# Kernel tuning notes

Hardware: AMD Instinct MI355X
Metric: run time of the kernel (lower is better)

## Reference

```python
import jax, jax.numpy as jnp
import numpy as np

NUM_HEADS = 16

def _stablemax3_s(x):
    # 3rd-order Taylor approx of exp(x), Eq 38
    pos = 1.0 + x * (1.0 + 0.5 * x * (1.0 + x / 3.0))
    neg = 1.0 / (1.0 - x * (1.0 - 0.5 * x * (1.0 - x / 3.0)))
    return jnp.where(x >= 0, pos, neg)

def stablemax3(logits, axis=-1):
    logits = logits - jnp.max(logits, axis=axis, keepdims=True)
    s = _stablemax3_s(logits)
    return s / jnp.sum(s, axis=axis, keepdims=True)

def setup_inputs() -> dict:
    key = jax.random.key(0)
    k1, k2, k3 = jax.random.split(key, 3)
    B, S, D = 2, 2048, 1024
    x = jax.random.normal(k1, (B, S, D), dtype=jnp.float32)
    w_qkv = jax.random.normal(k2, (3 * D, D), dtype=jnp.float32) * 0.02
    w_out = jax.random.normal(k3, (D, D), dtype=jnp.float32) * 0.02
    b_out = jnp.zeros((D,), dtype=jnp.float32)
    return {"x": x, "w_qkv": w_qkv, "w_out": w_out, "b_out": b_out}

def reference(x, w_qkv, w_out, b_out):
    B, S, D = x.shape
    H = NUM_HEADS
    hd = D // H
    scale = hd ** (-0.5)
    qkv = x @ w_qkv.T                                  # [B, S, 3D]
    qkv = qkv.reshape(B, S, 3, H, hd)
    qkv = jnp.transpose(qkv, (2, 0, 3, 1, 4))          # [3, B, H, S, hd]
    q, k, v = qkv[0], qkv[1], qkv[2]                   # pos(.) is identity here
    attn = jnp.einsum('bhsd,bhtd->bhst', q, k) * scale # [B, H, S, S]
    attn = stablemax3(attn, axis=-1)
    out = jnp.einsum('bhst,bhtd->bhsd', attn, v)       # [B, H, S, hd]
    out = jnp.transpose(out, (0, 2, 1, 3)).reshape(B, S, D)
    return out @ w_out.T + b_out
```

## Files before the change

kernel.cpp:

```cpp
#include <hip/hip_runtime.h>

typedef _Float16 half8 __attribute__((ext_vector_type(8)));
typedef _Float16 half4 __attribute__((ext_vector_type(4)));
typedef _Float16 half2v __attribute__((ext_vector_type(2)));
typedef float floatx4 __attribute__((ext_vector_type(4)));
typedef unsigned int uint2v __attribute__((ext_vector_type(2)));
typedef unsigned int uint4v __attribute__((ext_vector_type(4)));

__device__ __forceinline__ void gl_lds16(const _Float16* g, _Float16* l) {
    __builtin_amdgcn_global_load_lds(
        (const __attribute__((address_space(1))) void*)g,
        (__attribute__((address_space(3))) void*)l, 16, 0, 0);
}

__device__ __forceinline__ half2v cvt_pk(float a, float b) {
    return __builtin_bit_cast(half2v, __builtin_amdgcn_cvt_pkrtz(a, b));
}

__device__ __forceinline__ half2v rcp2(half2v d) {
#if __has_builtin(__builtin_amdgcn_rcph)
    half2v r;
    r[0] = __builtin_amdgcn_rcph(d[0]);
    r[1] = __builtin_amdgcn_rcph(d[1]);
    return r;
#else
    half2v r;
    r[0] = (_Float16)__builtin_amdgcn_rcpf((float)d[0]);
    r[1] = (_Float16)__builtin_amdgcn_rcpf((float)d[1]);
    return r;
#endif
}

__device__ __forceinline__ float dot2acc(half2v a, float acc) {
#if __has_builtin(__builtin_amdgcn_fdot2)
    const half2v one = {(_Float16)1.0f, (_Float16)1.0f};
    return __builtin_amdgcn_fdot2(a, one, acc, false);
#else
    return acc + (float)a[0] + (float)a[1];
#endif
}

__device__ __forceinline__ half8 from4(half2v a, half2v b, half2v c, half2v d) {
    uint4v u = {__builtin_bit_cast(unsigned int, a), __builtin_bit_cast(unsigned int, b),
                __builtin_bit_cast(unsigned int, c), __builtin_bit_cast(unsigned int, d)};
    return __builtin_bit_cast(half8, u);
}

__device__ __forceinline__ half8 from_lohi(half4 lo, half4 hi) {
    uint2v l = __builtin_bit_cast(uint2v, lo);
    uint2v h = __builtin_bit_cast(uint2v, hi);
    uint4v u = {l[0], l[1], h[0], h[1]};
    return __builtin_bit_cast(half8, u);
}

__global__ __launch_bounds__(256) void cvt_xw(const floatx4* __restrict__ x,
                                              const floatx4* __restrict__ wq,
                                              half4* __restrict__ xh,
                                              half4* __restrict__ wqh) {
    int i = blockIdx.x * 256 + threadIdx.x;
    floatx4 v;
    half4 h;
    if (i < 1048576) {
        v = x[i];
#pragma unroll
        for (int j = 0; j < 4; ++j) h[j] = (_Float16)v[j];
        xh[i] = h;
    } else {
        int j4 = i - 1048576;
        v = wq[j4];
#pragma unroll
        for (int j = 0; j < 4; ++j) h[j] = (_Float16)v[j];
        wqh[j4] = h;
    }
}

__global__ __launch_bounds__(256) void cvt_f32_f16(const floatx4* __restrict__ in,
                                                   half4* __restrict__ out, int n4) {
    int i = blockIdx.x * 256 + threadIdx.x;
    if (i >= n4) return;
    floatx4 v = in[i];
    half4 h;
#pragma unroll
    for (int j = 0; j < 4; ++j) h[j] = (_Float16)v[j];
    out[i] = h;
}

__global__ __launch_bounds__(256) void gemm_qkv(const _Float16* __restrict__ A,
                                                const _Float16* __restrict__ B,
                                                _Float16* __restrict__ qh,
                                                _Float16* __restrict__ kh,
                                                _Float16* __restrict__ vth) {
    const int K = 1024;
    __shared__ _Float16 SH[128 * 68];
    _Float16* As = SH;
    _Float16* Bs = SH + 4096;
    const int t = threadIdx.x;
    const int lane = t & 63, w = t >> 6;
    const int l15 = lane & 15, quad = lane >> 4;
    const int wm = w >> 1, wn = w & 1;
    const int m0 = blockIdx.y * 128, n0 = blockIdx.x * 128;

    floatx4 acc[4][4];
    const floatx4 zf = {0.f, 0.f, 0.f, 0.f};
#pragma unroll
    for (int i = 0; i < 4; ++i)
#pragma unroll
        for (int j = 0; j < 4; ++j) acc[i][j] = zf;

    for (int kt = 0; kt < K; kt += 32) {
        __syncthreads();
#pragma unroll
        for (int it = 0; it < 2; ++it) {
            int cc = it * 256 + t;
            int row = cc >> 2, kc = cc & 3;
            gl_lds16(&A[(size_t)(m0 + row) * K + kt + kc * 8], &As[cc * 8]);
            gl_lds16(&B[(size_t)(n0 + row) * K + kt + kc * 8], &Bs[cc * 8]);
        }
        __syncthreads();
        half8 af[4], bfr[4];
#pragma unroll
        for (int i = 0; i < 4; ++i)
            af[i] = *(const half8*)&As[(wm * 64 + i * 16 + l15) * 32 + quad * 8];
#pragma unroll
        for (int i = 0; i < 4; ++i)
            bfr[i] = *(const half8*)&Bs[(wn * 64 + i * 16 + l15) * 32 + quad * 8];
#pragma unroll
        for (int mi = 0; mi < 4; ++mi)
#pragma unroll
            for (int ni = 0; ni < 4; ++ni)
                acc[mi][ni] = __builtin_amdgcn_mfma_f32_16x16x32_f16(af[mi], bfr[ni],
                                                                     acc[mi][ni], 0, 0, 0);
    }

    const int b = m0 >> 11, s0 = m0 & 2047;
#pragma unroll
    for (int hf = 0; hf < 2; ++hf) {
        __syncthreads();
        if (wn == hf) {
#pragma unroll
            for (int mi = 0; mi < 4; ++mi)
#pragma unroll
                for (int ni = 0; ni < 4; ++ni)
#pragma unroll
                    for (int r = 0; r < 4; ++r)
                        SH[(wm * 64 + mi * 16 + quad * 4 + r) * 68 + ni * 16 + l15] =
                            (_Float16)acc[mi][ni][r];
        }
        __syncthreads();
        const int cbase = n0 + hf * 64;
        if (n0 < 2048) {
            const int hh = (cbase & 1023) >> 6;
            _Float16* dst = (n0 < 1024 ? qh : kh) + (size_t)((b << 4) | hh) * 131072;
#pragma unroll
            for (int it = 0; it < 4; ++it) {
                int cc = it * 256 + t;
                int r = cc >> 3, c8 = cc & 7;
                half4 lo = *(const half4*)&SH[r * 68 + c8 * 8];
                half4 hi = *(const half4*)&SH[r * 68 + c8 * 8 + 4];
                *(half8*)&dst[(size_t)(s0 + r) * 64 + c8 * 8] = from_lohi(lo, hi);
            }
        } else {
            const int hh = (cbase - 2048) >> 6;
            _Float16* dst = vth + (size_t)((b << 4) | hh) * 131072;
#pragma unroll
            for (int it = 0; it < 4; ++it) {
                int cc = it * 256 + t;
                int d = cc >> 4, s8 = cc & 15;
                half8 v;
#pragma unroll
                for (int j = 0; j < 8; ++j) v[j] = SH[(s8 * 8 + j) * 68 + d];
                *(half8*)&dst[(size_t)d * 2048 + s0 + s8 * 8] = v;
            }
        }
    }
}

__global__ __launch_bounds__(256) void gemm_out(const _Float16* __restrict__ A,
                                                const _Float16* __restrict__ B,
                                                float* __restrict__ C,
                                                const float* __restrict__ bias) {
    const int K = 1024, N = 1024;
    __shared__ _Float16 SH[6144];
    _Float16* As = SH;
    _Float16* Bs = SH + 2048;
    const int t = threadIdx.x;
    const int lane = t & 63, w = t >> 6;
    const int l15 = lane & 15, quad = lane >> 4;
    const int wm = w >> 1, wn = w & 1;
    const int m0 = blockIdx.y * 64, n0 = blockIdx.x * 128;

    floatx4 acc[2][4];
    const floatx4 zf = {0.f, 0.f, 0.f, 0.f};
#pragma unroll
    for (int i = 0; i < 2; ++i)
#pragma unroll
        for (int j = 0; j < 4; ++j) acc[i][j] = zf;

    for (int kt = 0; kt < K; kt += 32) {
        __syncthreads();
        {
            int row = t >> 2, kc = t & 3;
            gl_lds16(&A[(size_t)(m0 + row) * K + kt + kc * 8], &As[t * 8]);
        }
#pragma unroll
        for (int it = 0; it < 2; ++it) {
            int cc = it * 256 + t;
            int row = cc >> 2, kc = cc & 3;
            gl_lds16(&B[(size_t)(n0 + row) * K + kt + kc * 8], &Bs[cc * 8]);
        }
        __syncthreads();
        half8 af[2], bfr[4];
#pragma unroll
        for (int i = 0; i < 2; ++i)
            af[i] = *(const half8*)&As[(wm * 32 + i * 16 + l15) * 32 + quad * 8];
#pragma unroll
        for (int i = 0; i < 4; ++i)
            bfr[i] = *(const half8*)&Bs[(wn * 64 + i * 16 + l15) * 32 + quad * 8];
#pragma unroll
        for (int mi = 0; mi < 2; ++mi)
#pragma unroll
            for (int ni = 0; ni < 4; ++ni)
                acc[mi][ni] = __builtin_amdgcn_mfma_f32_16x16x32_f16(af[mi], bfr[ni],
                                                                     acc[mi][ni], 0, 0, 0);
    }

#pragma unroll
    for (int mi = 0; mi < 2; ++mi) {
#pragma unroll
        for (int ni = 0; ni < 4; ++ni) {
            int col = n0 + wn * 64 + ni * 16 + l15;
            float bv = bias[col];
#pragma unroll
            for (int r = 0; r < 4; ++r) {
                int row = m0 + wm * 32 + mi * 16 + quad * 4 + r;
                C[(size_t)row * N + col] = acc[mi][ni][r] + bv;
            }
        }
    }
}

__global__ __launch_bounds__(256) void attn_kernel(const _Float16* __restrict__ qh,
                                                   const _Float16* __restrict__ kh,
                                                   const _Float16* __restrict__ vth,
                                                   _Float16* __restrict__ out) {
    __shared__ _Float16 SM[16384];

    const int t = threadIdx.x;
    const int lane = t & 63, w = t >> 6;
    const int l15 = lane & 15, quad = lane >> 4;
    const int sw = l15 & 7;
    const int q0 = blockIdx.x * 128;
    const int bh = blockIdx.y;
    const int b = bh >> 4, h = bh & 15;

    const _Float16* Qp = qh + (size_t)bh * 131072 + q0 * 64;
    const _Float16* Kp = kh + (size_t)bh * 131072;
    const _Float16* VTp = vth + (size_t)bh * 131072;

    const int row0 = t >> 3, cg0 = (t & 7) ^ (row0 & 7);
    const int row1 = 32 + row0, cg1 = (t & 7) ^ (row1 & 7);
    const _Float16* K0 = &Kp[(size_t)row0 * 64 + cg0 * 8];
    const _Float16* K1 = &Kp[(size_t)row1 * 64 + cg1 * 8];
    const _Float16* V0 = &VTp[(size_t)row0 * 2048 + cg0 * 8];
    const _Float16* V1 = &VTp[(size_t)row1 * 2048 + cg1 * 8];

    const floatx4 zf = {0.f, 0.f, 0.f, 0.f};

    half8 qf[2][2];
#pragma unroll
    for (int nh = 0; nh < 2; ++nh)
#pragma unroll
        for (int kk = 0; kk < 2; ++kk) {
            half8 q = *(const half8*)&Qp[(w * 32 + nh * 16 + l15) * 64 + kk * 32 + quad * 8];
#pragma unroll
            for (int j = 0; j < 8; ++j) q[j] = q[j] * (_Float16)0.125f;
            qf[nh][kk] = q;
        }

    float rmax[2] = {-1.0e30f, -1.0e30f};
    gl_lds16(K0, &SM[t * 8]);
    gl_lds16(K1, &SM[2048 + t * 8]);
    __syncthreads();
    for (int kt = 0, cur = 0; kt < 2048; kt += 64, cur ^= 1) {
        if (kt + 64 < 2048) {
            _Float16* kd = cur ? &SM[0] : &SM[4096];
            gl_lds16(K0 + (size_t)(kt + 64) * 64, kd + t * 8);
            gl_lds16(K1 + (size_t)(kt + 64) * 64, kd + 2048 + t * 8);
        }
        const _Float16* Ks = cur ? &SM[4096] : &SM[0];
        floatx4 sa[4][2];
#pragma unroll
        for (int T = 0; T < 4; ++T) { sa[T][0] = zf; sa[T][1] = zf; }
#pragma unroll
        for (int kk = 0; kk < 2; ++kk) {
            half8 kf[4];
#pragma unroll
            for (int T = 0; T < 4; ++T)
                kf[T] = *(const half8*)&Ks[((T * 16 + l15) << 6) +
                                           ((((kk << 2) + quad) ^ sw) << 3)];
            __builtin_amdgcn_s_setprio(1);
#pragma unroll
            for (int T = 0; T < 4; ++T)
#pragma unroll
                for (int nh = 0; nh < 2; ++nh)
                    sa[T][nh] = __builtin_amdgcn_mfma_f32_16x16x32_f16(kf[T], qf[nh][kk],
                                                                      sa[T][nh], 0, 0, 0);
            __builtin_amdgcn_s_setprio(0);
        }
#pragma unroll
        for (int T = 0; T < 4; ++T)
#pragma unroll
            for (int nh = 0; nh < 2; ++nh)
#pragma unroll
                for (int r = 0; r < 4; ++r)
                    rmax[nh] = fmaxf(rmax[nh], sa[T][nh][r]);
        __syncthreads();
    }
#pragma unroll
    for (int nh = 0; nh < 2; ++nh) {
        rmax[nh] = fmaxf(rmax[nh], __shfl_xor(rmax[nh], 16, 64));
        rmax[nh] = fmaxf(rmax[nh], __shfl_xor(rmax[nh], 32, 64));
    }
    const floatx4 xmv[2] = {{-rmax[0], -rmax[0], -rmax[0], -rmax[0]},
                            {-rmax[1], -rmax[1], -rmax[1], -rmax[1]}};

    const half2v cA = {(_Float16)(-1.0f / 6.0f), (_Float16)(-1.0f / 6.0f)};
    const half2v cB = {(_Float16)0.5f, (_Float16)0.5f};
    const half2v cC = {(_Float16)-1.0f, (_Float16)-1.0f};
    const half2v cD = {(_Float16)1.0f, (_Float16)1.0f};

    float rsum[2] = {0.f, 0.f};
    floatx4 oacc[4][2];
#pragma unroll
    for (int i = 0; i < 4; ++i) { oacc[i][0] = zf; oacc[i][1] = zf; }

    gl_lds16(K0, &SM[t * 8]);
    gl_lds16(K1, &SM[2048 + t * 8]);
    gl_lds16(V0, &SM[8192 + t * 8]);
    gl_lds16(V1, &SM[8192 + 2048 + t * 8]);
    __syncthreads();
    for (int kt = 0, cur = 0; kt < 2048; kt += 64, cur ^= 1) {
        if (kt + 64 < 2048) {
            _Float16* kd = cur ? &SM[0] : &SM[4096];
            _Float16* vd = cur ? &SM[8192] : &SM[12288];
            gl_lds16(K0 + (size_t)(kt + 64) * 64, kd + t * 8);
            gl_lds16(K1 + (size_t)(kt + 64) * 64, kd + 2048 + t * 8);
            gl_lds16(V0 + (kt + 64), vd + t * 8);
            gl_lds16(V1 + (kt + 64), vd + 2048 + t * 8);
        }
        const _Float16* Ks = cur ? &SM[4096] : &SM[0];
        const _Float16* VTs = cur ? &SM[12288] : &SM[8192];

        floatx4 sa[4][2];
#pragma unroll
        for (int T = 0; T < 4; ++T) { sa[T][0] = xmv[0]; sa[T][1] = xmv[1]; }
#pragma unroll
        for (int kk = 0; kk < 2; ++kk) {
            half8 kf[4];
#pragma unroll
            for (int T = 0; T < 4; ++T)
                kf[T] = *(const half8*)&Ks[((T * 16 + l15) << 6) +
                                           ((((kk << 2) + quad) ^ sw) << 3)];
            __builtin_amdgcn_s_setprio(1);
#pragma unroll
            for (int T = 0; T < 4; ++T)
#pragma unroll
                for (int nh = 0; nh < 2; ++nh)
                    sa[T][nh] = __builtin_amdgcn_mfma_f32_16x16x32_f16(kf[T], qf[nh][kk],
                                                                      sa[T][nh], 0, 0, 0);
            __builtin_amdgcn_s_setprio(0);
        }
#pragma unroll
        for (int c = 0; c < 2; ++c) {
            half8 vf[4];
#pragma unroll
            for (int di = 0; di < 4; ++di) {
                const int bl = (di * 16 + l15) << 6;
                const int clo = (((c << 2) + (quad >> 1)) ^ sw) << 3;
                const int chi = (((c << 2) + 2 + (quad >> 1)) ^ sw) << 3;
                half4 lo = *(const half4*)&VTs[bl + clo + ((quad & 1) << 2)];
                half4 hi = *(const half4*)&VTs[bl + chi + ((quad & 1) << 2)];
                vf[di] = from_lohi(lo, hi);
            }
#pragma unroll
            for (int nh = 0; nh < 2; ++nh) {
                half2v p2m[4];
#pragma unroll
                for (int m = 0; m < 4; ++m) {
                    int T = 2 * c + (m >> 1);
                    int r0 = (m & 1) * 2;
                    half2v x2 = cvt_pk(sa[T][nh][r0], sa[T][nh][r0 + 1]);
                    half2v hp = __builtin_elementwise_fma(x2, cA, cB);
                    hp = __builtin_elementwise_fma(x2, hp, cC);
                    hp = __builtin_elementwise_fma(x2, hp, cD);
                    half2v p2 = rcp2(hp);
                    rsum[nh] = dot2acc(p2, rsum[nh]);
                    p2m[m] = p2;
                }
                half8 pb = from4(p2m[0], p2m[1], p2m[2], p2m[3]);
                __builtin_amdgcn_s_setprio(1);
#pragma unroll
                for (int di = 0; di < 4; ++di)
                    oacc[di][nh] = __builtin_amdgcn_mfma_f32_16x16x32_f16(vf[di], pb,
                                                                         oacc[di][nh], 0, 0, 0);
                __builtin_amdgcn_s_setprio(0);
            }
        }
        __syncthreads();
    }

#pragma unroll
    for (int nh = 0; nh < 2; ++nh) {
        rsum[nh] += __shfl_xor(rsum[nh], 16, 64);
        rsum[nh] += __shfl_xor(rsum[nh], 32, 64);
    }
    const float inv[2] = {1.0f / rsum[0], 1.0f / rsum[1]};

    _Float16* Os = SM;
#pragma unroll
    for (int di = 0; di < 4; ++di) {
#pragma unroll
        for (int nh = 0; nh < 2; ++nh) {
            half4 hv;
#pragma unroll
            for (int r = 0; r < 4; ++r) hv[r] = (_Float16)(oacc[di][nh][r] * inv[nh]);
            *(half4*)&Os[(w * 32 + nh * 16 + l15) * 72 + di * 16 + quad * 4] = hv;
        }
    }
    __syncthreads();
    _Float16* Op = out + (size_t)(b * 2048 + q0) * 1024 + h * 64;
#pragma unroll
    for (int it = 0; it < 4; ++it) {
        int cc = it * 256 + t;
        int r = cc >> 3, c8 = cc & 7;
        *(half8*)&Op[(size_t)r * 1024 + c8 * 8] = *(const half8*)&Os[r * 72 + c8 * 8];
    }
}

extern "C" void kernel_launch(void* const* d_in, const int* in_sizes, int n_in,
                              void* d_out, int out_size, void* d_ws, size_t ws_size,
                              hipStream_t stream) {
    const float* x_f = (const float*)d_in[0];
    const float* wqkv_f = (const float*)d_in[1];
    const float* wout_f = (const float*)d_in[2];
    const float* bias_f = (const float*)d_in[3];

    char* ws = (char*)d_ws;
    _Float16* xh = (_Float16*)(ws);
    _Float16* aoh = xh;
    _Float16* wqh = (_Float16*)(ws + 8388608);
    _Float16* woh = wqh;
    _Float16* qh = (_Float16*)(ws + 14680064);
    _Float16* kh = (_Float16*)(ws + 23068672);
    _Float16* vth = (_Float16*)(ws + 31457280);

    cvt_xw<<<7168, 256, 0, stream>>>((const floatx4*)x_f, (const floatx4*)wqkv_f,
                                     (half4*)xh, (half4*)wqh);
    gemm_qkv<<<dim3(24, 32), 256, 0, stream>>>(xh, wqh, qh, kh, vth);
    cvt_f32_f16<<<1024, 256, 0, stream>>>((const floatx4*)wout_f, (half4*)woh, 262144);
    attn_kernel<<<dim3(16, 32), 256, 0, stream>>>(qh, kh, vth, aoh);
    gemm_out<<<dim3(8, 64), 256, 0, stream>>>(aoh, woh, (float*)d_out, bias_f);
}
```

Baseline: 213.7 us.

## Split attention key tiles across wave pairs and halve query rows per block

Each attention block now handles 64 query rows instead of 128. Its four waves form two query groups by two key halves, with each wave covering half of every 64-key tile. The row max and the partial output and row-sum accumulators are merged through LDS at the end, and the grid doubles to 1024 blocks with a launch-bounds hint for 4 blocks per CU. The aim is more blocks to fill the CUs and fewer registers per wave. The cost is that each block now streams the full K and V for only half as many queries, so global and LDS traffic per query roughly doubles, plus extra syncs for the cross-wave reductions.

```diff
diff --git a/kernel.cpp b/kernel.cpp
--- a/kernel.cpp
+++ b/kernel.cpp
@@ -239,17 +239,18 @@
     }
 }
 
-__global__ __launch_bounds__(256) void attn_kernel(const _Float16* __restrict__ qh,
-                                                   const _Float16* __restrict__ kh,
-                                                   const _Float16* __restrict__ vth,
-                                                   _Float16* __restrict__ out) {
+__global__ __launch_bounds__(256, 4) void attn_kernel(const _Float16* __restrict__ qh,
+                                                      const _Float16* __restrict__ kh,
+                                                      const _Float16* __restrict__ vth,
+                                                      _Float16* __restrict__ out) {
     __shared__ _Float16 SM[16384];
 
     const int t = threadIdx.x;
     const int lane = t & 63, w = t >> 6;
     const int l15 = lane & 15, quad = lane >> 4;
     const int sw = l15 & 7;
-    const int q0 = blockIdx.x * 128;
+    const int qg = w >> 1, kg = w & 1;
+    const int q0 = blockIdx.x * 64;
     const int bh = blockIdx.y;
     const int b = bh >> 4, h = bh & 15;
 
@@ -258,11 +259,10 @@
     const _Float16* VTp = vth + (size_t)bh * 131072;
 
     const int row0 = t >> 3, cg0 = (t & 7) ^ (row0 & 7);
-    const int row1 = 32 + row0, cg1 = (t & 7) ^ (row1 & 7);
     const _Float16* K0 = &Kp[(size_t)row0 * 64 + cg0 * 8];
-    const _Float16* K1 = &Kp[(size_t)row1 * 64 + cg1 * 8];
+    const _Float16* K1 = &Kp[(size_t)(32 + row0) * 64 + cg0 * 8];
     const _Float16* V0 = &VTp[(size_t)row0 * 2048 + cg0 * 8];
-    const _Float16* V1 = &VTp[(size_t)row1 * 2048 + cg1 * 8];
+    const _Float16* V1 = &VTp[(size_t)(32 + row0) * 2048 + cg0 * 8];
 
     const floatx4 zf = {0.f, 0.f, 0.f, 0.f};
 
@@ -271,7 +271,7 @@
     for (int nh = 0; nh < 2; ++nh)
 #pragma unroll
         for (int kk = 0; kk < 2; ++kk) {
-            half8 q = *(const half8*)&Qp[(w * 32 + nh * 16 + l15) * 64 + kk * 32 + quad * 8];
+            half8 q = *(const half8*)&Qp[(qg * 32 + nh * 16 + l15) * 64 + kk * 32 + quad * 8];
 #pragma unroll
             for (int j = 0; j < 8; ++j) q[j] = q[j] * (_Float16)0.125f;
             qf[nh][kk] = q;
@@ -288,38 +288,52 @@
             gl_lds16(K1 + (size_t)(kt + 64) * 64, kd + 2048 + t * 8);
         }
         const _Float16* Ks = cur ? &SM[4096] : &SM[0];
-        floatx4 sa[4][2];
-#pragma unroll
-        for (int T = 0; T < 4; ++T) { sa[T][0] = zf; sa[T][1] = zf; }
+        floatx4 sa[2][2];
+#pragma unroll
+        for (int Ti = 0; Ti < 2; ++Ti) { sa[Ti][0] = zf; sa[Ti][1] = zf; }
 #pragma unroll
         for (int kk = 0; kk < 2; ++kk) {
-            half8 kf[4];
-#pragma unroll
-            for (int T = 0; T < 4; ++T)
-                kf[T] = *(const half8*)&Ks[((T * 16 + l15) << 6) +
-                                           ((((kk << 2) + quad) ^ sw) << 3)];
+            half8 kf[2];
+#pragma unroll
+            for (int Ti = 0; Ti < 2; ++Ti)
+                kf[Ti] = *(const half8*)&Ks[(((kg * 2 + Ti) * 16 + l15) << 6) +
+                                            ((((kk << 2) + quad) ^ sw) << 3)];
             __builtin_amdgcn_s_setprio(1);
 #pragma unroll
-            for (int T = 0; T < 4; ++T)
+            for (int Ti = 0; Ti < 2; ++Ti)
 #pragma unroll
                 for (int nh = 0; nh < 2; ++nh)
-                    sa[T][nh] = __builtin_amdgcn_mfma_f32_16x16x32_f16(kf[T], qf[nh][kk],
-                                                                      sa[T][nh], 0, 0, 0);
+                    sa[Ti][nh] = __builtin_amdgcn_mfma_f32_16x16x32_f16(kf[Ti], qf[nh][kk],
+                                                                        sa[Ti][nh], 0, 0, 0);
             __builtin_amdgcn_s_setprio(0);
         }
 #pragma unroll
-        for (int T = 0; T < 4; ++T)
+        for (int Ti = 0; Ti < 2; ++Ti)
 #pragma unroll
             for (int nh = 0; nh < 2; ++nh)
 #pragma unroll
                 for (int r = 0; r < 4; ++r)
-                    rmax[nh] = fmaxf(rmax[nh], sa[T][nh][r]);
+                    rmax[nh] = fmaxf(rmax[nh], sa[Ti][nh][r]);
         __syncthreads();
     }
 #pragma unroll
     for (int nh = 0; nh < 2; ++nh) {
         rmax[nh] = fmaxf(rmax[nh], __shfl_xor(rmax[nh], 16, 64));
         rmax[nh] = fmaxf(rmax[nh], __shfl_xor(rmax[nh], 32, 64));
+    }
+    {
+        float* EXM = (float*)SM;
+        if (quad == 0) {
+#pragma unroll
+            for (int nh = 0; nh < 2; ++nh)
+                EXM[((qg * 2 + nh) * 2 + kg) * 16 + l15] = rmax[nh];
+        }
+        __syncthreads();
+#pragma unroll
+        for (int nh = 0; nh < 2; ++nh)
+            rmax[nh] = fmaxf(EXM[((qg * 2 + nh) * 2 + 0) * 16 + l15],
+                             EXM[((qg * 2 + nh) * 2 + 1) * 16 + l15]);
+        __syncthreads();
     }
     const floatx4 xmv[2] = {{-rmax[0], -rmax[0], -rmax[0], -rmax[0]},
                             {-rmax[1], -rmax[1], -rmax[1], -rmax[1]}};
@@ -351,60 +365,57 @@
         const _Float16* Ks = cur ? &SM[4096] : &SM[0];
         const _Float16* VTs = cur ? &SM[12288] : &SM[8192];
 
-        floatx4 sa[4][2];
-#pragma unroll
-        for (int T = 0; T < 4; ++T) { sa[T][0] = xmv[0]; sa[T][1] = xmv[1]; }
+        floatx4 sa[2][2];
+#pragma unroll
+        for (int Ti = 0; Ti < 2; ++Ti) { sa[Ti][0] = xmv[0]; sa[Ti][1] = xmv[1]; }
 #pragma unroll
         for (int kk = 0; kk < 2; ++kk) {
-            half8 kf[4];
-#pragma unroll
-            for (int T = 0; T < 4; ++T)
-                kf[T] = *(const half8*)&Ks[((T * 16 + l15) << 6) +
-                                           ((((kk << 2) + quad) ^ sw) << 3)];
+            half8 kf[2];
+#pragma unroll
+            for (int Ti = 0; Ti < 2; ++Ti)
+                kf[Ti] = *(const half8*)&Ks[(((kg * 2 + Ti) * 16 + l15) << 6) +
+                                            ((((kk << 2) + quad) ^ sw) << 3)];
             __builtin_amdgcn_s_setprio(1);
 #pragma unroll
-            for (int T = 0; T < 4; ++T)
+            for (int Ti = 0; Ti < 2; ++Ti)
 #pragma unroll
                 for (int nh = 0; nh < 2; ++nh)
-                    sa[T][nh] = __builtin_amdgcn_mfma_f32_16x16x32_f16(kf[T], qf[nh][kk],
-                                                                      sa[T][nh], 0, 0, 0);
+                    sa[Ti][nh] = __builtin_amdgcn_mfma_f32_16x16x32_f16(kf[Ti], qf[nh][kk],
+                                                                        sa[Ti][nh], 0, 0, 0);
             __builtin_amdgcn_s_setprio(0);
         }
-#pragma unroll
-        for (int c = 0; c < 2; ++c) {
-            half8 vf[4];
-#pragma unroll
-            for (int di = 0; di < 4; ++di) {
-                const int bl = (di * 16 + l15) << 6;
-                const int clo = (((c << 2) + (quad >> 1)) ^ sw) << 3;
-                const int chi = (((c << 2) + 2 + (quad >> 1)) ^ sw) << 3;
-                half4 lo = *(const half4*)&VTs[bl + clo + ((quad & 1) << 2)];
-                half4 hi = *(const half4*)&VTs[bl + chi + ((quad & 1) << 2)];
-                vf[di] = from_lohi(lo, hi);
+        half8 vf[4];
+#pragma unroll
+        for (int di = 0; di < 4; ++di) {
+            const int bl = (di * 16 + l15) << 6;
+            const int clo = (((kg << 2) + (quad >> 1)) ^ sw) << 3;
+            const int chi = (((kg << 2) + 2 + (quad >> 1)) ^ sw) << 3;
+            half4 lo = *(const half4*)&VTs[bl + clo + ((quad & 1) << 2)];
+            half4 hi = *(const half4*)&VTs[bl + chi + ((quad & 1) << 2)];
+            vf[di] = from_lohi(lo, hi);
+        }
+#pragma unroll
+        for (int nh = 0; nh < 2; ++nh) {
+            half2v p2m[4];
+#pragma unroll
+            for (int m = 0; m < 4; ++m) {
+                int Ti = m >> 1;
+                int r0 = (m & 1) * 2;
+                half2v x2 = cvt_pk(sa[Ti][nh][r0], sa[Ti][nh][r0 + 1]);
+                half2v hp = __builtin_elementwise_fma(x2, cA, cB);
+                hp = __builtin_elementwise_fma(x2, hp, cC);
+                hp = __builtin_elementwise_fma(x2, hp, cD);
+                half2v p2 = rcp2(hp);
+                rsum[nh] = dot2acc(p2, rsum[nh]);
+                p2m[m] = p2;
             }
-#pragma unroll
-            for (int nh = 0; nh < 2; ++nh) {
-                half2v p2m[4];
-#pragma unroll
-                for (int m = 0; m < 4; ++m) {
-                    int T = 2 * c + (m >> 1);
-                    int r0 = (m & 1) * 2;
-                    half2v x2 = cvt_pk(sa[T][nh][r0], sa[T][nh][r0 + 1]);
-                    half2v hp = __builtin_elementwise_fma(x2, cA, cB);
-                    hp = __builtin_elementwise_fma(x2, hp, cC);
-                    hp = __builtin_elementwise_fma(x2, hp, cD);
-                    half2v p2 = rcp2(hp);
-                    rsum[nh] = dot2acc(p2, rsum[nh]);
-                    p2m[m] = p2;
-                }
-                half8 pb = from4(p2m[0], p2m[1], p2m[2], p2m[3]);
-                __builtin_amdgcn_s_setprio(1);
-#pragma unroll
-                for (int di = 0; di < 4; ++di)
-                    oacc[di][nh] = __builtin_amdgcn_mfma_f32_16x16x32_f16(vf[di], pb,
-                                                                         oacc[di][nh], 0, 0, 0);
-                __builtin_amdgcn_s_setprio(0);
-            }
+            half8 pb = from4(p2m[0], p2m[1], p2m[2], p2m[3]);
+            __builtin_amdgcn_s_setprio(1);
+#pragma unroll
+            for (int di = 0; di < 4; ++di)
+                oacc[di][nh] = __builtin_amdgcn_mfma_f32_16x16x32_f16(vf[di], pb,
+                                                                      oacc[di][nh], 0, 0, 0);
+            __builtin_amdgcn_s_setprio(0);
         }
         __syncthreads();
     }
@@ -414,23 +425,46 @@
         rsum[nh] += __shfl_xor(rsum[nh], 16, 64);
         rsum[nh] += __shfl_xor(rsum[nh], 32, 64);
     }
-    const float inv[2] = {1.0f / rsum[0], 1.0f / rsum[1]};
-
-    _Float16* Os = SM;
-#pragma unroll
-    for (int di = 0; di < 4; ++di) {
-#pragma unroll
-        for (int nh = 0; nh < 2; ++nh) {
-            half4 hv;
-#pragma unroll
-            for (int r = 0; r < 4; ++r) hv[r] = (_Float16)(oacc[di][nh][r] * inv[nh]);
-            *(half4*)&Os[(w * 32 + nh * 16 + l15) * 72 + di * 16 + quad * 4] = hv;
-        }
+
+    float* EXO = (float*)SM;
+    float* EXS = (float*)(SM + 8192);
+    _Float16* Os = SM + 8320;
+    if (kg) {
+#pragma unroll
+        for (int nh = 0; nh < 2; ++nh)
+#pragma unroll
+            for (int di = 0; di < 4; ++di)
+                *(floatx4*)&EXO[(((((qg * 2 + nh) * 4 + di) * 4 + quad) * 16) + l15) * 4] =
+                    oacc[di][nh];
+        if (quad == 0) {
+#pragma unroll
+            for (int nh = 0; nh < 2; ++nh)
+                EXS[(qg * 2 + nh) * 16 + l15] = rsum[nh];
+        }
+    }
+    __syncthreads();
+    if (!kg) {
+        float inv[2];
+#pragma unroll
+        for (int nh = 0; nh < 2; ++nh)
+            inv[nh] = 1.0f / (rsum[nh] + EXS[(qg * 2 + nh) * 16 + l15]);
+#pragma unroll
+        for (int nh = 0; nh < 2; ++nh)
+#pragma unroll
+            for (int di = 0; di < 4; ++di) {
+                floatx4 part = *(const floatx4*)
+                    &EXO[(((((qg * 2 + nh) * 4 + di) * 4 + quad) * 16) + l15) * 4];
+                half4 hv;
+#pragma unroll
+                for (int r = 0; r < 4; ++r)
+                    hv[r] = (_Float16)((oacc[di][nh][r] + part[r]) * inv[nh]);
+                *(half4*)&Os[(qg * 32 + nh * 16 + l15) * 72 + di * 16 + quad * 4] = hv;
+            }
     }
     __syncthreads();
     _Float16* Op = out + (size_t)(b * 2048 + q0) * 1024 + h * 64;
 #pragma unroll
-    for (int it = 0; it < 4; ++it) {
+    for (int it = 0; it < 2; ++it) {
         int cc = it * 256 + t;
         int r = cc >> 3, c8 = cc & 7;
         *(half8*)&Op[(size_t)r * 1024 + c8 * 8] = *(const half8*)&Os[r * 72 + c8 * 8];
@@ -458,6 +492,6 @@
                                      (half4*)xh, (half4*)wqh);
     gemm_qkv<<<dim3(24, 32), 256, 0, stream>>>(xh, wqh, qh, kh, vth);
     cvt_f32_f16<<<1024, 256, 0, stream>>>((const floatx4*)wout_f, (half4*)woh, 262144);
-    attn_kernel<<<dim3(16, 32), 256, 0, stream>>>(qh, kh, vth, aoh);
+    attn_kernel<<<dim3(32, 32), 256, 0, stream>>>(qh, kh, vth, aoh);
     gemm_out<<<dim3(8, 64), 256, 0, stream>>>(aoh, woh, (float*)d_out, bias_f);
 }
```

After: 213.1 us. Within noise of the previous version (-0.3%).
